# Optimization experiments

Hardware: AMD Instinct MI355X
Metric: run time of the kernel (lower is better)

## Reference

```python
import jax, jax.numpy as jnp
import numpy as np
from math import sqrt


def setup_inputs() -> dict:
    key = jax.random.key(0)
    kq, kk, kv = jax.random.split(key, 3)
    B, L, H, E = 4, 2048, 8, 64
    S, D = L, E
    return {
        "queries": jax.random.normal(kq, (B, L, H, E), dtype=jnp.float32),
        "keys": jax.random.normal(kk, (B, S, H, E), dtype=jnp.float32),
        "values": jax.random.normal(kv, (B, S, H, D), dtype=jnp.float32),
    }


def reference(queries, keys, values):
    # FullAttention with mask_flag=True (TriangularCausalMask), dropout p=0,
    # output_attention=False. scale = 1/sqrt(E).
    B, L, H, E = queries.shape
    S = keys.shape[1]
    scale = 1.0 / sqrt(E)
    # scores: [B, H, L, S]
    scores = jnp.einsum("blhe,bshe->bhls", queries, keys)
    # causal mask: positions s > l are masked (upper triangle above diagonal)
    causal = jnp.tril(jnp.ones((L, S), dtype=bool))  # True = keep
    neg_inf = jnp.finfo(scores.dtype).min
    scores = jnp.where(causal, scores, neg_inf)
    A = jax.nn.softmax(scale * scores, axis=-1)  # [B,H,L,S]
    # context: [B, L, H, D]
    V = jnp.einsum("bhls,bshd->blhd", A, values)
    return V
```

## Files before the change

kernel.cpp:

```cpp
#include <hip/hip_runtime.h>
#include <math.h>

#define BD 4
#define LD 2048
#define HD 8
#define ED 64
#define TQ 64
#define TK 64
#define RS (HD * ED)
#define NT 32
#define TILE_BYTES 8192

typedef __attribute__((ext_vector_type(8))) _Float16 f16x8;
typedef __attribute__((ext_vector_type(4))) _Float16 f16x4;
typedef __attribute__((ext_vector_type(4))) float f32x4;
typedef __attribute__((ext_vector_type(4))) unsigned int u32x4;
typedef __attribute__((ext_vector_type(2))) unsigned int u32x2;
typedef unsigned int u32;
typedef unsigned long long u64;

__device__ inline u32 pkh(float a, float b) {
    return __builtin_bit_cast(u32, __builtin_amdgcn_cvt_pkrtz(a, b));
}
__device__ inline u64 pkh4(float a, float b, float c, float d) {
    return (u64)pkh(a, b) | ((u64)pkh(c, d) << 32);
}
__device__ inline int swz(int row, int bcol) {
    return row * 128 + ((((bcol >> 4) ^ row) & 7) << 4) + (bcol & 15);
}

__global__ __launch_bounds__(256, 4)
void cvt_kv(const float* __restrict__ K, const float* __restrict__ V,
            char* __restrict__ Kimg, char* __restrict__ Vimg) {
    const int t  = threadIdx.x;
    const int b  = blockIdx.x >> 3;
    const int h  = blockIdx.x & 7;
    const int kt = blockIdx.y;

    const int ks  = t >> 2;
    const int ke0 = (t & 3) << 2;
    const int vs0 = (t & 15) << 2;
    const int vd0 = (t >> 4) << 2;

    const size_t tb = ((size_t)((b * HD + h) * NT + kt)) * TILE_BYTES;
    char* kd = Kimg + tb;
    char* vd = Vimg + tb;

    const float* kp = K + ((size_t)((b * LD + kt * TK + ks) * HD + h)) * ED + ke0;
    const float* vp = V + ((size_t)((b * LD + kt * TK + vs0) * HD + h)) * ED + vd0;

    float4 kx[4], vx[4];
    #pragma unroll
    for (int j = 0; j < 4; ++j) kx[j] = *(const float4*)(kp + 16 * j);
    #pragma unroll
    for (int r = 0; r < 4; ++r) vx[r] = *(const float4*)(vp + r * RS);

    #pragma unroll
    for (int j = 0; j < 4; ++j)
        *(u64*)(kd + swz(ks, 2 * (ke0 + 16 * j))) = pkh4(kx[j].x, kx[j].y, kx[j].z, kx[j].w);
    *(u64*)(vd + swz(vd0 + 0, 2 * vs0)) = pkh4(vx[0].x, vx[1].x, vx[2].x, vx[3].x);
    *(u64*)(vd + swz(vd0 + 1, 2 * vs0)) = pkh4(vx[0].y, vx[1].y, vx[2].y, vx[3].y);
    *(u64*)(vd + swz(vd0 + 2, 2 * vs0)) = pkh4(vx[0].z, vx[1].z, vx[2].z, vx[3].z);
    *(u64*)(vd + swz(vd0 + 3, 2 * vs0)) = pkh4(vx[0].w, vx[1].w, vx[2].w, vx[3].w);
}

__global__ __launch_bounds__(256, 2)
void fa_f16img(const char* __restrict__ Kimg, const char* __restrict__ Vimg,
               const float* __restrict__ Q, float* __restrict__ O) {
    __shared__ __align__(16) char smem[33792];

    const int t    = threadIdx.x;
    const int lane = t & 63;
    const int w    = t >> 6;
    const int m16  = lane & 15;
    const int quad = lane >> 4;

    const int b = blockIdx.x >> 3;
    const int h = blockIdx.x & 7;
    const int y  = (int)blockIdx.y;
    const int r  = y & 7;
    const int c  = y >> 3;
    const int qt = (c == 0) ? (31 - r) : (c == 1) ? (r + 8)
                 : (c == 2) ? (23 - r) : r;
    const int q0  = qt * TQ;
    const int len = qt + 1;

    const char* Kt = Kimg + (size_t)(b * HD + h) * NT * TILE_BYTES;
    const char* Vt = Vimg + (size_t)(b * HD + h) * NT * TILE_BYTES;

    const int swK0 = swz((w << 4) + m16, quad * 16);
    const int swK1 = swz((w << 4) + m16, 64 + quad * 16);
    int swV[4];
    #pragma unroll
    for (int dt = 0; dt < 4; ++dt)
        swV[dt] = swz(dt * 16 + m16, (w << 5) + (quad << 3));

    const float qscale = 0.125f * 1.44269504088896340736f;
    f16x8 qf[4][2];
    #pragma unroll
    for (int qs = 0; qs < 4; ++qs) {
        const float* qrow =
            Q + ((size_t)((b * LD + q0 + (qs << 4) + m16) * HD + h)) * ED;
        #pragma unroll
        for (int hf = 0; hf < 2; ++hf) {
            const float4 x  = *(const float4*)(qrow + hf * 32 + quad * 8);
            const float4 y4 = *(const float4*)(qrow + hf * 32 + quad * 8 + 4);
            u32x4 p;
            p[0] = pkh(x.x * qscale, x.y * qscale);
            p[1] = pkh(x.z * qscale, x.w * qscale);
            p[2] = pkh(y4.x * qscale, y4.y * qscale);
            p[3] = pkh(y4.z * qscale, y4.w * qscale);
            qf[qs][hf] = __builtin_bit_cast(f16x8, p);
        }
    }

    f32x4 oacc[4][4];
    float l_i[4] = {0.f, 0.f, 0.f, 0.f};
    #pragma unroll
    for (int dt = 0; dt < 4; ++dt)
        #pragma unroll
        for (int qs = 0; qs < 4; ++qs) oacc[dt][qs] = (f32x4){0.f, 0.f, 0.f, 0.f};

    f16x8 kc0 = *(const f16x8*)(Kt + swK0);
    f16x8 kc1 = *(const f16x8*)(Kt + swK1);
    f16x4 vc[4];
    #pragma unroll
    for (int dt = 0; dt < 4; ++dt)
        vc[dt] = *(const f16x4*)(Vt + swV[dt]);

    for (int kt = 0; kt < len; ++kt) {
        const int ktn = (kt + 1 < len) ? (kt + 1) : kt;
        const char* kb = Kt + (size_t)ktn * TILE_BYTES;
        const char* vb = Vt + (size_t)ktn * TILE_BYTES;
        f16x8 kn0 = *(const f16x8*)(kb + swK0);
        f16x8 kn1 = *(const f16x8*)(kb + swK1);
        f16x4 vn[4];
        #pragma unroll
        for (int dt = 0; dt < 4; ++dt)
            vn[dt] = *(const f16x4*)(vb + swV[dt]);
        __builtin_amdgcn_sched_barrier(0);

        const bool diag = (kt == qt);
        #pragma unroll
        for (int qs = 0; qs < 4; ++qs) {
            f32x4 z = {0.f, 0.f, 0.f, 0.f};
            z = __builtin_amdgcn_mfma_f32_16x16x32_f16(kc0, qf[qs][0], z, 0, 0, 0);
            z = __builtin_amdgcn_mfma_f32_16x16x32_f16(kc1, qf[qs][1], z, 0, 0, 0);

            if (diag) {
                const int ql = (qs << 4) + m16;
                const int sl = (w << 4) + (quad << 2);
                #pragma unroll
                for (int i = 0; i < 4; ++i)
                    if (sl + i > ql) z[i] = -INFINITY;
            }

            float p0 = __builtin_amdgcn_exp2f(z[0]);
            float p1 = __builtin_amdgcn_exp2f(z[1]);
            float p2 = __builtin_amdgcn_exp2f(z[2]);
            float p3 = __builtin_amdgcn_exp2f(z[3]);
            l_i[qs] += (p0 + p1) + (p2 + p3);
            u32x2 pp;
            pp[0] = pkh(p0, p1);
            pp[1] = pkh(p2, p3);
            const f16x4 pf = __builtin_bit_cast(f16x4, pp);

            #pragma unroll
            for (int dt = 0; dt < 4; ++dt)
                oacc[dt][qs] = __builtin_amdgcn_mfma_f32_16x16x16f16(vc[dt], pf, oacc[dt][qs], 0, 0, 0);
        }

        kc0 = kn0;
        kc1 = kn1;
        #pragma unroll
        for (int dt = 0; dt < 4; ++dt) vc[dt] = vn[dt];
    }

    #pragma unroll
    for (int qs = 0; qs < 4; ++qs) {
        float l = l_i[qs];
        l += __shfl_xor(l, 16);
        l += __shfl_xor(l, 32);
        l_i[qs] = l;
    }
    float* lbuf = (float*)(smem + 32768);
    if (quad == 0) {
        #pragma unroll
        for (int qs = 0; qs < 4; ++qs)
            lbuf[(w << 6) + (qs << 4) + m16] = l_i[qs];
    }
    if (w >= 2) {
        char* reg = smem + ((w - 2) << 14);
        #pragma unroll
        for (int dt = 0; dt < 4; ++dt)
            #pragma unroll
            for (int qs = 0; qs < 4; ++qs)
                *(f32x4*)(reg + ((((dt << 2) | qs)) << 10) + (lane << 4)) = oacc[dt][qs];
    }
    __syncthreads();
    if (w < 2) {
        char* reg = smem + (w << 14);
        #pragma unroll
        for (int dt = 0; dt < 4; ++dt)
            #pragma unroll
            for (int qs = 0; qs < 4; ++qs)
                oacc[dt][qs] += *(const f32x4*)(reg + ((((dt << 2) | qs)) << 10) + (lane << 4));
    }
    __syncthreads();
    if (w == 1) {
        char* reg = smem;
        #pragma unroll
        for (int dt = 0; dt < 4; ++dt)
            #pragma unroll
            for (int qs = 0; qs < 4; ++qs)
                *(f32x4*)(reg + ((((dt << 2) | qs)) << 10) + (lane << 4)) = oacc[dt][qs];
    }
    __syncthreads();
    if (w == 0) {
        char* reg = smem;
        float inv[4];
        #pragma unroll
        for (int qs = 0; qs < 4; ++qs)
            inv[qs] = 1.0f / (lbuf[(qs << 4) + m16] + lbuf[64 + (qs << 4) + m16] +
                              lbuf[128 + (qs << 4) + m16] + lbuf[192 + (qs << 4) + m16]);
        #pragma unroll
        for (int dt = 0; dt < 4; ++dt)
            #pragma unroll
            for (int qs = 0; qs < 4; ++qs)
                oacc[dt][qs] += *(const f32x4*)(reg + ((((dt << 2) | qs)) << 10) + (lane << 4));
        #pragma unroll
        for (int qs = 0; qs < 4; ++qs) {
            float* orow =
                O + ((size_t)((b * LD + q0 + (qs << 4) + m16) * HD + h)) * ED;
            #pragma unroll
            for (int dt = 0; dt < 4; ++dt) {
                float4 o;
                o.x = oacc[dt][qs][0] * inv[qs];
                o.y = oacc[dt][qs][1] * inv[qs];
                o.z = oacc[dt][qs][2] * inv[qs];
                o.w = oacc[dt][qs][3] * inv[qs];
                *(float4*)(orow + dt * 16 + (quad << 2)) = o;
            }
        }
    }
}

__global__ __launch_bounds__(256, 4)
void fa_mfma_q64(const float* __restrict__ Q, const float* __restrict__ K,
                 const float* __restrict__ V, float* __restrict__ O) {
    __shared__ __align__(16) char smem[32768];
    const int t = threadIdx.x, lane = t & 63, w = t >> 6;
    const int m16 = lane & 15, quad = lane >> 4;
    const int b = blockIdx.x >> 3, h = blockIdx.x & 7;
    const int y = (int)blockIdx.y, r = y & 7, c = y >> 3;
    const int qt = (c == 0) ? (31 - r) : (c == 1) ? (r + 8) : (c == 2) ? (23 - r) : r;
    const int q0 = qt * TQ;
    const int len = qt + 1;
    const int ks = t >> 2, ke0 = (t & 3) << 2;
    const int vs0 = (t & 15) << 2, vd0 = (t >> 4) << 2;
    const float* Kbase = K + ((size_t)((b * LD + ks) * HD + h)) * ED + ke0;
    const float* Vbase = V + ((size_t)((b * LD + vs0) * HD + h)) * ED + vd0;
    const float qscale = 0.125f * 1.44269504088896340736f;
    f16x8 qf[2];
    {
        const float* qrow = Q + ((size_t)((b * LD + q0 + (w << 4) + m16) * HD + h)) * ED;
        #pragma unroll
        for (int hf = 0; hf < 2; ++hf) {
            const float4 x = *(const float4*)(qrow + hf * 32 + quad * 8);
            const float4 y4 = *(const float4*)(qrow + hf * 32 + quad * 8 + 4);
            u32x4 p;
            p[0] = pkh(x.x * qscale, x.y * qscale);
            p[1] = pkh(x.z * qscale, x.w * qscale);
            p[2] = pkh(y4.x * qscale, y4.y * qscale);
            p[3] = pkh(y4.z * qscale, y4.w * qscale);
            qf[hf] = __builtin_bit_cast(f16x8, p);
        }
    }
    f32x4 oacc[4];
    float l_i = 0.0f;
    #pragma unroll
    for (int nt = 0; nt < 4; ++nt) oacc[nt] = (f32x4){0.f, 0.f, 0.f, 0.f};
    float4 kx[4], vx[4];
    {
        #pragma unroll
        for (int j = 0; j < 4; ++j) kx[j] = *(const float4*)(Kbase + 16 * j);
        #pragma unroll
        for (int rr = 0; rr < 4; ++rr) vx[rr] = *(const float4*)(Vbase + rr * RS);
        char* wK = smem;
        char* wV = smem + 16384;
        #pragma unroll
        for (int j = 0; j < 4; ++j)
            *(u64*)(wK + swz(ks, 2 * (ke0 + 16 * j))) = pkh4(kx[j].x, kx[j].y, kx[j].z, kx[j].w);
        *(u64*)(wV + swz(vd0 + 0, 2 * vs0)) = pkh4(vx[0].x, vx[1].x, vx[2].x, vx[3].x);
        *(u64*)(wV + swz(vd0 + 1, 2 * vs0)) = pkh4(vx[0].y, vx[1].y, vx[2].y, vx[3].y);
        *(u64*)(wV + swz(vd0 + 2, 2 * vs0)) = pkh4(vx[0].z, vx[1].z, vx[2].z, vx[3].z);
        *(u64*)(wV + swz(vd0 + 3, 2 * vs0)) = pkh4(vx[0].w, vx[1].w, vx[2].w, vx[3].w);
    }
    __syncthreads();
    for (int kt = 0; kt < len; ++kt) {
        char* rK = smem + ((kt & 1) << 13);
        char* rV = smem + 16384 + ((kt & 1) << 13);
        const bool pre = kt < len - 1;
        if (pre) {
            const float* kp = Kbase + (size_t)(kt + 1) * (TK * RS);
            const float* vp = Vbase + (size_t)(kt + 1) * (TK * RS);
            #pragma unroll
            for (int j = 0; j < 4; ++j) kx[j] = *(const float4*)(kp + 16 * j);
            #pragma unroll
            for (int rr = 0; rr < 4; ++rr) vx[rr] = *(const float4*)(vp + rr * RS);
        }
        f32x4 sacc[4];
        #pragma unroll
        for (int kc = 0; kc < 4; ++kc) {
            const f16x8 kf0 = *(const f16x8*)(rK + swz(kc * 16 + m16, quad * 16));
            const f16x8 kf1 = *(const f16x8*)(rK + swz(kc * 16 + m16, 64 + quad * 16));
            f32x4 z = {0.f, 0.f, 0.f, 0.f};
            z = __builtin_amdgcn_mfma_f32_16x16x32_f16(kf0, qf[0], z, 0, 0, 0);
            z = __builtin_amdgcn_mfma_f32_16x16x32_f16(kf1, qf[1], z, 0, 0, 0);
            sacc[kc] = z;
        }
        if (kt == qt) {
            const int ql = (w << 4) + m16;
            #pragma unroll
            for (int kc = 0; kc < 4; ++kc)
                #pragma unroll
                for (int i = 0; i < 4; ++i)
                    if (kc * 16 + quad * 4 + i > ql) sacc[kc][i] = -INFINITY;
        }
        f16x4 pf[4];
        #pragma unroll
        for (int kc = 0; kc < 4; ++kc) {
            float p0 = __builtin_amdgcn_exp2f(sacc[kc][0]);
            float p1 = __builtin_amdgcn_exp2f(sacc[kc][1]);
            float p2 = __builtin_amdgcn_exp2f(sacc[kc][2]);
            float p3 = __builtin_amdgcn_exp2f(sacc[kc][3]);
            l_i += (p0 + p1) + (p2 + p3);
            u32x2 pp;
            pp[0] = pkh(p0, p1);
            pp[1] = pkh(p2, p3);
            pf[kc] = __builtin_bit_cast(f16x4, pp);
        }
        #pragma unroll
        for (int kc = 0; kc < 4; ++kc) {
            #pragma unroll
            for (int dt = 0; dt < 4; ++dt) {
                const f16x4 vf = *(const f16x4*)
                    (rV + swz(dt * 16 + m16, 2 * (kc * 16 + quad * 4)));
                oacc[dt] = __builtin_amdgcn_mfma_f32_16x16x16f16(vf, pf[kc], oacc[dt], 0, 0, 0);
            }
        }
        if (pre) {
            char* wK = smem + ((kt & 1) ? 0 : 8192);
            char* wV = smem + 16384 + ((kt & 1) ? 0 : 8192);
            #pragma unroll
            for (int j = 0; j < 4; ++j)
                *(u64*)(wK + swz(ks, 2 * (ke0 + 16 * j))) = pkh4(kx[j].x, kx[j].y, kx[j].z, kx[j].w);
            *(u64*)(wV + swz(vd0 + 0, 2 * vs0)) = pkh4(vx[0].x, vx[1].x, vx[2].x, vx[3].x);
            *(u64*)(wV + swz(vd0 + 1, 2 * vs0)) = pkh4(vx[0].y, vx[1].y, vx[2].y, vx[3].y);
            *(u64*)(wV + swz(vd0 + 2, 2 * vs0)) = pkh4(vx[0].z, vx[1].z, vx[2].z, vx[3].z);
            *(u64*)(wV + swz(vd0 + 3, 2 * vs0)) = pkh4(vx[0].w, vx[1].w, vx[2].w, vx[3].w);
        }
        __syncthreads();
    }
    {
        float l = l_i;
        l += __shfl_xor(l, 16);
        l += __shfl_xor(l, 32);
        const float inv = 1.0f / l;
        float* orow = O + ((size_t)((b * LD + q0 + (w << 4) + m16) * HD + h)) * ED;
        #pragma unroll
        for (int dt = 0; dt < 4; ++dt) {
            float4 o;
            o.x = oacc[dt][0] * inv;
            o.y = oacc[dt][1] * inv;
            o.z = oacc[dt][2] * inv;
            o.w = oacc[dt][3] * inv;
            *(float4*)(orow + dt * 16 + quad * 4) = o;
        }
    }
}

extern "C" void kernel_launch(void* const* d_in, const int* in_sizes, int n_in,
                              void* d_out, int out_size, void* d_ws, size_t ws_size,
                              hipStream_t stream) {
    const float* Q = (const float*)d_in[0];
    const float* K = (const float*)d_in[1];
    const float* V = (const float*)d_in[2];
    float* O = (float*)d_out;

    const size_t img = (size_t)BD * HD * NT * TILE_BYTES;
    if (d_ws != nullptr && ws_size >= 2 * img) {
        char* Kimg = (char*)d_ws;
        char* Vimg = (char*)d_ws + img;
        cvt_kv<<<dim3(BD * HD, NT), 256, 0, stream>>>(K, V, Kimg, Vimg);
        fa_f16img<<<dim3(BD * HD, 32), 256, 0, stream>>>(Kimg, Vimg, Q, O);
    } else {
        fa_mfma_q64<<<dim3(BD * HD, 32), 256, 0, stream>>>(Q, K, V, O);
    }
}
```

Measured before the change: 123.0 us.

## Fold paired causal query tiles into one 512-thread block for balanced work

Each block now handles two query tiles, f and 31-f, in sequence, so every block does the same 33 key-tile iterations and causal work is balanced. Block size doubles to 8 waves split into two groups of 32 query rows each, with K/V tiles shared across groups. The grid halves to 16 per head. Between the two tiles a shared-memory reduction, with its extra barriers, runs mid-loop before the second Q tile is reloaded.

```diff
diff --git a/kernel.cpp b/kernel.cpp
--- a/kernel.cpp
+++ b/kernel.cpp
@@ -64,62 +64,133 @@
     *(u64*)(vd + swz(vd0 + 3, 2 * vs0)) = pkh4(vx[0].w, vx[1].w, vx[2].w, vx[3].w);
 }
 
-__global__ __launch_bounds__(256, 2)
-void fa_f16img(const char* __restrict__ Kimg, const char* __restrict__ Vimg,
-               const float* __restrict__ Q, float* __restrict__ O) {
+__global__ __launch_bounds__(512, 2)
+void fa_fold(const char* __restrict__ Kimg, const char* __restrict__ Vimg,
+             const float* __restrict__ Q, float* __restrict__ O) {
     __shared__ __align__(16) char smem[33792];
 
     const int t    = threadIdx.x;
     const int lane = t & 63;
     const int w    = t >> 6;
+    const int g    = w >> 2;
+    const int ws   = w & 3;
     const int m16  = lane & 15;
     const int quad = lane >> 4;
 
     const int b = blockIdx.x >> 3;
     const int h = blockIdx.x & 7;
-    const int y  = (int)blockIdx.y;
-    const int r  = y & 7;
-    const int c  = y >> 3;
-    const int qt = (c == 0) ? (31 - r) : (c == 1) ? (r + 8)
-                 : (c == 2) ? (23 - r) : r;
-    const int q0  = qt * TQ;
-    const int len = qt + 1;
+    const int f = (int)blockIdx.y;
 
     const char* Kt = Kimg + (size_t)(b * HD + h) * NT * TILE_BYTES;
     const char* Vt = Vimg + (size_t)(b * HD + h) * NT * TILE_BYTES;
 
-    const int swK0 = swz((w << 4) + m16, quad * 16);
-    const int swK1 = swz((w << 4) + m16, 64 + quad * 16);
+    const int swK0 = swz((ws << 4) + m16, quad * 16);
+    const int swK1 = swz((ws << 4) + m16, 64 + quad * 16);
     int swV[4];
     #pragma unroll
     for (int dt = 0; dt < 4; ++dt)
-        swV[dt] = swz(dt * 16 + m16, (w << 5) + (quad << 3));
+        swV[dt] = swz(dt * 16 + m16, (ws << 5) + (quad << 3));
 
     const float qscale = 0.125f * 1.44269504088896340736f;
-    f16x8 qf[4][2];
-    #pragma unroll
-    for (int qs = 0; qs < 4; ++qs) {
-        const float* qrow =
-            Q + ((size_t)((b * LD + q0 + (qs << 4) + m16) * HD + h)) * ED;
-        #pragma unroll
-        for (int hf = 0; hf < 2; ++hf) {
-            const float4 x  = *(const float4*)(qrow + hf * 32 + quad * 8);
-            const float4 y4 = *(const float4*)(qrow + hf * 32 + quad * 8 + 4);
-            u32x4 p;
-            p[0] = pkh(x.x * qscale, x.y * qscale);
-            p[1] = pkh(x.z * qscale, x.w * qscale);
-            p[2] = pkh(y4.x * qscale, y4.y * qscale);
-            p[3] = pkh(y4.z * qscale, y4.w * qscale);
-            qf[qs][hf] = __builtin_bit_cast(f16x8, p);
-        }
-    }
-
-    f32x4 oacc[4][4];
-    float l_i[4] = {0.f, 0.f, 0.f, 0.f};
+    f16x8 qf[2][2];
+    auto loadQ = [&](int qtile) {
+        #pragma unroll
+        for (int qs = 0; qs < 2; ++qs) {
+            const float* qrow = Q +
+                ((size_t)((b * LD + qtile * TQ + (g << 5) + (qs << 4) + m16) * HD + h)) * ED;
+            #pragma unroll
+            for (int hf = 0; hf < 2; ++hf) {
+                const float4 x  = *(const float4*)(qrow + hf * 32 + quad * 8);
+                const float4 y4 = *(const float4*)(qrow + hf * 32 + quad * 8 + 4);
+                u32x4 p;
+                p[0] = pkh(x.x * qscale, x.y * qscale);
+                p[1] = pkh(x.z * qscale, x.w * qscale);
+                p[2] = pkh(y4.x * qscale, y4.y * qscale);
+                p[3] = pkh(y4.z * qscale, y4.w * qscale);
+                qf[qs][hf] = __builtin_bit_cast(f16x8, p);
+            }
+        }
+    };
+    loadQ(f);
+
+    f32x4 oacc[4][2];
+    float l_i[2] = {0.f, 0.f};
     #pragma unroll
     for (int dt = 0; dt < 4; ++dt)
         #pragma unroll
-        for (int qs = 0; qs < 4; ++qs) oacc[dt][qs] = (f32x4){0.f, 0.f, 0.f, 0.f};
+        for (int qs = 0; qs < 2; ++qs) oacc[dt][qs] = (f32x4){0.f, 0.f, 0.f, 0.f};
+
+    auto reduce_store = [&](int qtile) {
+        #pragma unroll
+        for (int qs = 0; qs < 2; ++qs) {
+            float l = l_i[qs];
+            l += __shfl_xor(l, 16);
+            l += __shfl_xor(l, 32);
+            l_i[qs] = l;
+        }
+        float* lbuf = (float*)(smem + 32768);
+        if (quad == 0) {
+            #pragma unroll
+            for (int qs = 0; qs < 2; ++qs)
+                lbuf[(g << 7) + (ws << 5) + (qs << 4) + m16] = l_i[qs];
+        }
+        if (ws >= 2) {
+            char* reg = smem + (((g << 1) | (ws - 2)) << 13);
+            #pragma unroll
+            for (int dt = 0; dt < 4; ++dt)
+                #pragma unroll
+                for (int qs = 0; qs < 2; ++qs)
+                    *(f32x4*)(reg + (((dt << 1) | qs) << 10) + (lane << 4)) = oacc[dt][qs];
+        }
+        __syncthreads();
+        if (ws < 2) {
+            char* reg = smem + (((g << 1) | ws) << 13);
+            #pragma unroll
+            for (int dt = 0; dt < 4; ++dt)
+                #pragma unroll
+                for (int qs = 0; qs < 2; ++qs)
+                    oacc[dt][qs] += *(const f32x4*)(reg + (((dt << 1) | qs) << 10) + (lane << 4));
+        }
+        __syncthreads();
+        if (ws == 1) {
+            char* reg = smem + ((g << 1) << 13);
+            #pragma unroll
+            for (int dt = 0; dt < 4; ++dt)
+                #pragma unroll
+                for (int qs = 0; qs < 2; ++qs)
+                    *(f32x4*)(reg + (((dt << 1) | qs) << 10) + (lane << 4)) = oacc[dt][qs];
+        }
+        __syncthreads();
+        if (ws == 0) {
+            char* reg = smem + ((g << 1) << 13);
+            float inv[2];
+            #pragma unroll
+            for (int qs = 0; qs < 2; ++qs) {
+                const int o = (g << 7) + (qs << 4) + m16;
+                inv[qs] = 1.0f / (lbuf[o] + lbuf[o + 32] + lbuf[o + 64] + lbuf[o + 96]);
+            }
+            #pragma unroll
+            for (int dt = 0; dt < 4; ++dt)
+                #pragma unroll
+                for (int qs = 0; qs < 2; ++qs)
+                    oacc[dt][qs] += *(const f32x4*)(reg + (((dt << 1) | qs) << 10) + (lane << 4));
+            #pragma unroll
+            for (int qs = 0; qs < 2; ++qs) {
+                float* orow = O +
+                    ((size_t)((b * LD + qtile * TQ + (g << 5) + (qs << 4) + m16) * HD + h)) * ED;
+                #pragma unroll
+                for (int dt = 0; dt < 4; ++dt) {
+                    float4 o;
+                    o.x = oacc[dt][qs][0] * inv[qs];
+                    o.y = oacc[dt][qs][1] * inv[qs];
+                    o.z = oacc[dt][qs][2] * inv[qs];
+                    o.w = oacc[dt][qs][3] * inv[qs];
+                    *(float4*)(orow + dt * 16 + (quad << 2)) = o;
+                }
+            }
+        }
+        __syncthreads();
+    };
 
     f16x8 kc0 = *(const f16x8*)(Kt + swK0);
     f16x8 kc1 = *(const f16x8*)(Kt + swK1);
@@ -128,8 +199,12 @@
     for (int dt = 0; dt < 4; ++dt)
         vc[dt] = *(const f16x4*)(Vt + swV[dt]);
 
-    for (int kt = 0; kt < len; ++kt) {
-        const int ktn = (kt + 1 < len) ? (kt + 1) : kt;
+    for (int i = 0; i <= 32; ++i) {
+        const int kt    = (i <= f) ? i : (32 - i);
+        const int qtile = (i <= f) ? f : (31 - f);
+
+        int ktn = (i < f) ? (i + 1) : (31 - i);
+        if (ktn < 0) ktn = 0;
         const char* kb = Kt + (size_t)ktn * TILE_BYTES;
         const char* vb = Vt + (size_t)ktn * TILE_BYTES;
         f16x8 kn0 = *(const f16x8*)(kb + swK0);
@@ -140,19 +215,19 @@
             vn[dt] = *(const f16x4*)(vb + swV[dt]);
         __builtin_amdgcn_sched_barrier(0);
 
-        const bool diag = (kt == qt);
-        #pragma unroll
-        for (int qs = 0; qs < 4; ++qs) {
+        const bool diag = (kt == qtile);
+        #pragma unroll
+        for (int qs = 0; qs < 2; ++qs) {
             f32x4 z = {0.f, 0.f, 0.f, 0.f};
             z = __builtin_amdgcn_mfma_f32_16x16x32_f16(kc0, qf[qs][0], z, 0, 0, 0);
             z = __builtin_amdgcn_mfma_f32_16x16x32_f16(kc1, qf[qs][1], z, 0, 0, 0);
 
             if (diag) {
-                const int ql = (qs << 4) + m16;
-                const int sl = (w << 4) + (quad << 2);
-                #pragma unroll
-                for (int i = 0; i < 4; ++i)
-                    if (sl + i > ql) z[i] = -INFINITY;
+                const int ql = (g << 5) + (qs << 4) + m16;
+                const int sl = (ws << 4) + (quad << 2);
+                #pragma unroll
+                for (int ii = 0; ii < 4; ++ii)
+                    if (sl + ii > ql) z[ii] = -INFINITY;
             }
 
             float p0 = __builtin_amdgcn_exp2f(z[0]);
@@ -170,79 +245,24 @@
                 oacc[dt][qs] = __builtin_amdgcn_mfma_f32_16x16x16f16(vc[dt], pf, oacc[dt][qs], 0, 0, 0);
         }
 
+        if (i == f) {
+            reduce_store(f);
+            #pragma unroll
+            for (int dt = 0; dt < 4; ++dt)
+                #pragma unroll
+                for (int qs = 0; qs < 2; ++qs) oacc[dt][qs] = (f32x4){0.f, 0.f, 0.f, 0.f};
+            l_i[0] = 0.f;
+            l_i[1] = 0.f;
+            loadQ(31 - f);
+        }
+
         kc0 = kn0;
         kc1 = kn1;
         #pragma unroll
         for (int dt = 0; dt < 4; ++dt) vc[dt] = vn[dt];
     }
 
-    #pragma unroll
-    for (int qs = 0; qs < 4; ++qs) {
-        float l = l_i[qs];
-        l += __shfl_xor(l, 16);
-        l += __shfl_xor(l, 32);
-        l_i[qs] = l;
-    }
-    float* lbuf = (float*)(smem + 32768);
-    if (quad == 0) {
-        #pragma unroll
-        for (int qs = 0; qs < 4; ++qs)
-            lbuf[(w << 6) + (qs << 4) + m16] = l_i[qs];
-    }
-    if (w >= 2) {
-        char* reg = smem + ((w - 2) << 14);
-        #pragma unroll
-        for (int dt = 0; dt < 4; ++dt)
-            #pragma unroll
-            for (int qs = 0; qs < 4; ++qs)
-                *(f32x4*)(reg + ((((dt << 2) | qs)) << 10) + (lane << 4)) = oacc[dt][qs];
-    }
-    __syncthreads();
-    if (w < 2) {
-        char* reg = smem + (w << 14);
-        #pragma unroll
-        for (int dt = 0; dt < 4; ++dt)
-            #pragma unroll
-            for (int qs = 0; qs < 4; ++qs)
-                oacc[dt][qs] += *(const f32x4*)(reg + ((((dt << 2) | qs)) << 10) + (lane << 4));
-    }
-    __syncthreads();
-    if (w == 1) {
-        char* reg = smem;
-        #pragma unroll
-        for (int dt = 0; dt < 4; ++dt)
-            #pragma unroll
-            for (int qs = 0; qs < 4; ++qs)
-                *(f32x4*)(reg + ((((dt << 2) | qs)) << 10) + (lane << 4)) = oacc[dt][qs];
-    }
-    __syncthreads();
-    if (w == 0) {
-        char* reg = smem;
-        float inv[4];
-        #pragma unroll
-        for (int qs = 0; qs < 4; ++qs)
-            inv[qs] = 1.0f / (lbuf[(qs << 4) + m16] + lbuf[64 + (qs << 4) + m16] +
-                              lbuf[128 + (qs << 4) + m16] + lbuf[192 + (qs << 4) + m16]);
-        #pragma unroll
-        for (int dt = 0; dt < 4; ++dt)
-            #pragma unroll
-            for (int qs = 0; qs < 4; ++qs)
-                oacc[dt][qs] += *(const f32x4*)(reg + ((((dt << 2) | qs)) << 10) + (lane << 4));
-        #pragma unroll
-        for (int qs = 0; qs < 4; ++qs) {
-            float* orow =
-                O + ((size_t)((b * LD + q0 + (qs << 4) + m16) * HD + h)) * ED;
-            #pragma unroll
-            for (int dt = 0; dt < 4; ++dt) {
-                float4 o;
-                o.x = oacc[dt][qs][0] * inv[qs];
-                o.y = oacc[dt][qs][1] * inv[qs];
-                o.z = oacc[dt][qs][2] * inv[qs];
-                o.w = oacc[dt][qs][3] * inv[qs];
-                *(float4*)(orow + dt * 16 + (quad << 2)) = o;
-            }
-        }
-    }
+    reduce_store(31 - f);
 }
 
 __global__ __launch_bounds__(256, 4)
@@ -393,7 +413,7 @@
         char* Kimg = (char*)d_ws;
         char* Vimg = (char*)d_ws + img;
         cvt_kv<<<dim3(BD * HD, NT), 256, 0, stream>>>(K, V, Kimg, Vimg);
-        fa_f16img<<<dim3(BD * HD, 32), 256, 0, stream>>>(Kimg, Vimg, Q, O);
+        fa_fold<<<dim3(BD * HD, 16), 512, 0, stream>>>(Kimg, Vimg, Q, O);
     } else {
         fa_mfma_q64<<<dim3(BD * HD, 32), 256, 0, stream>>>(Q, K, V, O);
     }
```

Result: slower. 137.0 us (+11.4%).
